# Optimization experiments

Hardware: AMD Instinct MI355X
Metric: run time of the kernel (lower is better)

## Reference

```python
import jax, jax.numpy as jnp
import numpy as np

HEADS = 6
K = 3       # kernel_size
PAD = 1     # padding (stride = 1, so AvgPool is identity and h=H, w=W)


def setup_inputs() -> dict:
    key = jax.random.key(0)
    ks = jax.random.split(key, 6)
    B, H, W, C = 8, 56, 56, 192
    k4h = (K ** 4) * HEADS  # 486
    s = 0.02
    return {
        "x":  jax.random.normal(ks[0], (B, H, W, C), jnp.float32),
        # weights stored as (in, out), i.e. transpose of torch nn.Linear.weight
        "Wv": jax.random.normal(ks[1], (C, C), jnp.float32) * s,
        "Wa": jax.random.normal(ks[2], (C, k4h), jnp.float32) * s,
        "ba": jnp.zeros((k4h,), jnp.float32),
        "Wp": jax.random.normal(ks[3], (C, C), jnp.float32) * s,
        "bp": jnp.zeros((C,), jnp.float32),
    }


def _outlook(x, Wv, Wa, ba, Wp, bp):
    B, H, W, C = x.shape
    hd = C // HEADS
    scale = hd ** (-0.5)
    k2 = K * K
    hw = H * W

    # v projection (no bias), to NCHW
    v = jnp.einsum("bhwc,cd->bdhw", x, Wv)                       # [B,C,H,W]

    # unfold: extract k x k local windows (same ordering as nn.Unfold: C, ki, kj)
    vp = jnp.pad(v, ((0, 0), (0, 0), (PAD, PAD), (PAD, PAD)))
    patches = jnp.stack(
        [vp[:, :, i:i + H, j:j + W] for i in range(K) for j in range(K)],
        axis=2,
    )                                                            # [B,C,k2,H,W]
    v = patches.reshape(B, HEADS, hd, k2, hw).transpose(0, 1, 4, 3, 2)  # [B,h,hw,k2,hd]

    # attention weights: dense predicted per location (pool is identity, stride=1)
    a = x.reshape(B, hw, C) @ Wa + ba                            # [B,hw,heads*k2*k2]
    a = a.reshape(B, hw, HEADS, k2, k2).transpose(0, 2, 1, 3, 4)  # [B,h,hw,k2,k2]
    a = jax.nn.softmax(a * scale, axis=-1)

    out = jnp.einsum("bnpkq,bnpqd->bnpkd", a, v)                 # [B,h,hw,k2,hd]

    # fold (col2im): scatter-add overlapping windows back, stride=1
    cols = out.transpose(0, 1, 4, 3, 2).reshape(B, C, K, K, H, W)
    acc = jnp.zeros((B, C, H + 2 * PAD, W + 2 * PAD), x.dtype)
    for i in range(K):
        for j in range(K):
            acc = acc.at[:, :, i:i + H, j:j + W].add(cols[:, :, i, j])
    y = acc[:, :, PAD:PAD + H, PAD:PAD + W].transpose(0, 2, 3, 1)  # [B,H,W,C]

    return y @ Wp + bp


def reference(x, Wv, Wa, ba, Wp, bp):
    return _outlook(x, Wv, Wa, ba, Wp, bp)
```

## Files before the change

### kernel.cpp

```cpp
#include <hip/hip_runtime.h>
#include <hip/hip_bf16.h>
#include <cstdint>

#define DI __device__ __forceinline__

typedef __attribute__((ext_vector_type(8))) short short8;
typedef __attribute__((ext_vector_type(4))) float f32x4;

DI float bflo(uint32_t u) { return __builtin_bit_cast(float, (uint32_t)(u << 16)); }
DI float bfhi(uint32_t u) { return __builtin_bit_cast(float, (uint32_t)(u & 0xffff0000u)); }
DI uint32_t cvtpk(float lo, float hi) {
    uint32_t r;
    asm("v_cvt_pk_bf16_f32 %0, %1, %2" : "=v"(r) : "v"(lo), "v"(hi));
    return r;
}
DI void gload16(const void* g, void* s) {
    __builtin_amdgcn_global_load_lds(
        (const __attribute__((address_space(1))) uint32_t*)g,
        (__attribute__((address_space(3))) uint32_t*)s, 16, 0, 0);
}
DI int xcd_swizzle(int orig, int nwg) {
    const int q = nwg >> 3, r = nwg & 7;
    const int x = orig & 7, i = orig >> 3;
    return (x < r ? x * (q + 1) : r * (q + 1) + (x - r) * q) + i;
}

constexpr int BATCH = 8, HH_IMG = 56, WW_IMG = 56, C = 192;
constexpr int HEADS = 6, HD = 32, NA = 486;
constexpr int NAP = 528;
constexpr int MROWS = BATCH * HH_IMG * WW_IMG;
constexpr int KK = 192;
constexpr int TILE_B  = 49152;
constexpr int PANEL_B = 49152;
constexpr int WTB_B   = 73728;

__global__ __launch_bounds__(256) void prep_all(const float* __restrict__ x,
                                                const float* __restrict__ Wv,
                                                const float* __restrict__ Wa,
                                                const float* __restrict__ Wp,
                                                const float* __restrict__ ba,
                                                uint8_t* __restrict__ xbf,
                                                uint8_t* __restrict__ WT,
                                                uint8_t* __restrict__ WTB,
                                                float* __restrict__ baP) {
    const int bid = blockIdx.x;
    if (bid < 2352) {
        const int g = bid * 256 + threadIdx.x;
        const int m = g / 24, cc = g % 24;
        const int ks = cc >> 2, lg = cc & 3;
        const float* src = x + (size_t)m * KK + cc * 8;
        const float4 v0 = *(const float4*)src;
        const float4 v1 = *(const float4*)(src + 4);
        uint4 o;
        o.x = cvtpk(v0.x, v0.y); o.y = cvtpk(v0.z, v0.w);
        o.z = cvtpk(v1.x, v1.y); o.w = cvtpk(v1.z, v1.w);
        const size_t off = (size_t)(m >> 7) * PANEL_B +
                           ((((m >> 4) & 7) * 6 + ks) * 64 + (lg << 4) + (m & 15)) * 16;
        *(uint4*)(xbf + off) = o;
        return;
    }
    const int tid = (bid - 2352) * 256 + threadIdx.x;
    if (tid < 18432) {
        const int s = tid % 24, rem = tid / 24;
        const int p = rem & 127, tile = rem >> 7;
        const int lc = (p >> 5) * 32 + 2 * (p & 15) + ((p >> 4) & 1);
        const int u  = tile * 128 + lc;
        const float* src = nullptr; int nc = 0, col = 0;
        if (u < 192) { src = Wv; nc = 192; col = u; }
        else if (u < 720) {
            const int up = u - 192;
            const int head = up / 88, r88 = up - head * 88;
            if (r88 < 81) { src = Wa; nc = NA; col = head * 81 + r88; }
        }
        const int k0 = s * 8;
        uint32_t d[4];
#pragma unroll
        for (int e = 0; e < 4; ++e) {
            const float f0 = src ? src[(size_t)(k0 + 2 * e) * nc + col]     : 0.f;
            const float f1 = src ? src[(size_t)(k0 + 2 * e + 1) * nc + col] : 0.f;
            d[e] = cvtpk(f0, f1);
        }
        const int sb = (s * 16) ^ ((p & 7) << 4);
        *(uint4*)(WT + (size_t)tile * TILE_B + p * 384 + sb) =
            make_uint4(d[0], d[1], d[2], d[3]);
    } else if (tid < 18432 + 4608) {
        const int g = tid - 18432;
        const int l = g & 63, gg = g >> 6;
        const int ks = gg % 6, nrIdx = gg / 6;
        const int pp = nrIdx >> 1, h = nrIdx & 1;
        const int col = pp * 32 + 2 * (l & 15) + h;
        const int k0  = ks * 32 + (l >> 4) * 8;
        uint32_t d[4];
#pragma unroll
        for (int e = 0; e < 4; ++e) {
            const float f0 = Wp[(size_t)(k0 + 2 * e) * 192 + col];
            const float f1 = Wp[(size_t)(k0 + 2 * e + 1) * 192 + col];
            d[e] = cvtpk(f0, f1);
        }
        *(uint4*)(WTB + (size_t)g * 16) = make_uint4(d[0], d[1], d[2], d[3]);
    } else if (tid < 18432 + 4608 + NAP) {
        const int pc = tid - 18432 - 4608;
        const int head = pc / 88, r88 = pc - head * 88;
        baP[pc] = (r88 < 81) ? ba[head * 81 + r88] : 0.f;
    }
}

__global__ __launch_bounds__(256, 2) void gemm_fr(
    const uint8_t* __restrict__ Afr,
    const uint8_t* __restrict__ WT,
    uint16_t* __restrict__ zOut, uint16_t* __restrict__ alogP,
    const float* __restrict__ baP) {
    __shared__ __align__(16) uint8_t sm[TILE_B];
    const int t    = threadIdx.x;
    const int wgid = xcd_swizzle(blockIdx.x, gridDim.x);
    const int mg   = wgid / 6, ti = wgid - mg * 6;
    const int m0   = mg * 128;
    const int l    = t & 63, wid = t >> 6;
    const int wr   = wid >> 1, wc = wid & 1;
    const int lr   = l & 15, lg = l >> 4;

    const uint8_t* wt = WT + (size_t)ti * TILE_B;
#pragma unroll
    for (int i = 0; i < 12; ++i) {
        const int off = wid * 12288 + i * 1024;
        gload16(wt + off + l * 16, sm + off);
    }

    const uint8_t* ap = Afr + (size_t)mg * PANEL_B;
    short8 aR[6][4];
#pragma unroll
    for (int ks = 0; ks < 6; ++ks)
#pragma unroll
        for (int mr = 0; mr < 4; ++mr) {
            const int r = wr * 4 + mr;
            aR[ks][mr] = *(const short8*)(ap + (size_t)(((r * 6 + ks) * 64) + l) * 16);
        }
    __syncthreads();

    f32x4 acc[4][4];
#pragma unroll
    for (int mr = 0; mr < 4; ++mr)
#pragma unroll
        for (int nr = 0; nr < 4; ++nr) acc[mr][nr] = f32x4{0.f, 0.f, 0.f, 0.f};
#pragma unroll
    for (int ks = 0; ks < 6; ++ks) {
        const int cb = ks * 64 + lg * 16;
        short8 b[4];
#pragma unroll
        for (int nr = 0; nr < 4; ++nr) {
            const int rn = wc * 64 + nr * 16 + lr;
            b[nr] = *(const short8*)(sm + rn * 384 + (cb ^ ((rn & 7) << 4)));
        }
#pragma unroll
        for (int mr = 0; mr < 4; ++mr)
#pragma unroll
            for (int nr = 0; nr < 4; ++nr)
                acc[mr][nr] = __builtin_amdgcn_mfma_f32_16x16x32_bf16(
                    aR[ks][mr], b[nr], acc[mr][nr], 0, 0, 0);
    }

    const int gcol0 = ti * 128 + wc * 64;
#pragma unroll
    for (int pr = 0; pr < 2; ++pr) {
        const int uc = gcol0 + pr * 32 + 2 * lr;
        if (uc < 192) {
#pragma unroll
            for (int mr = 0; mr < 4; ++mr) {
                const size_t rb = (size_t)(m0 + wr * 64 + mr * 16 + lg * 4);
#pragma unroll
                for (int j = 0; j < 4; ++j)
                    *(uint32_t*)(zOut + (rb + j) * 192 + uc) =
                        cvtpk(acc[mr][2 * pr][j], acc[mr][2 * pr + 1][j]);
            }
        } else {
            const int pc = uc - 192;
            if (pc < NAP) {
                const float be = baP[pc], bo = baP[pc + 1];
#pragma unroll
                for (int mr = 0; mr < 4; ++mr) {
                    const size_t rb = (size_t)(m0 + wr * 64 + mr * 16 + lg * 4);
#pragma unroll
                    for (int j = 0; j < 4; ++j)
                        *(uint32_t*)(alogP + (rb + j) * NAP + pc) =
                            cvtpk(acc[mr][2 * pr][j] + be, acc[mr][2 * pr + 1][j] + bo);
                }
            }
        }
    }
}

constexpr int TH = 4, TW = 8;
constexpr int HALO_W = TW + 4;
constexpr int HSTR = 80;
constexpr int PXSTR = HEADS * HSTR;
constexpr int VL_BYTES = 96 * PXSTR;

__global__ __launch_bounds__(192) void attn_fused(const uint16_t* __restrict__ z,
                                                  const uint16_t* __restrict__ alogP,
                                                  const uint8_t* __restrict__ WTB,
                                                  const float* __restrict__ bp,
                                                  float* __restrict__ out) {
    __shared__ __align__(16) uint8_t smem[VL_BYTES];
    const int b   = blockIdx.z;
    const int ty0 = blockIdx.y * TH, tx0 = blockIdx.x * TW;
    const int t   = threadIdx.x;

#pragma unroll
    for (int it = 0; it < 12; ++it) {
        const int f  = t + it * 192;
        const int px = f / 24, c8 = f % 24;
        const int hy = px / HALO_W, hx = px % HALO_W;
        const int y = ty0 + hy - 2, x = tx0 + hx - 2;
        uint4 val = make_uint4(0u, 0u, 0u, 0u);
        if ((unsigned)y < HH_IMG && (unsigned)x < WW_IMG)
            val = *(const uint4*)&z[(((size_t)b * HH_IMG + y) * WW_IMG + x) * C + c8 * 8];
        *(uint4*)(smem + px * PXSTR + (c8 >> 2) * HSTR + (c8 & 3) * 16) = val;
    }

    const int n   = t % HEADS, pxl = t / HEADS;
    const int py  = pxl >> 3, px_ = pxl & 7;
    const int Py  = ty0 + py, Px = tx0 + px_;
    const float scl2 = 0.17677669529663687f * 1.4426950408889634f;

    float cw[5][5] = {};
#pragma unroll
    for (int i = 0; i < 3; ++i)
#pragma unroll
        for (int j = 0; j < 3; ++j) {
            const int sy = Py - i + 1, sx = Px - j + 1;
            if ((unsigned)sy < HH_IMG && (unsigned)sx < WW_IMG) {
                const uint8_t* rp = (const uint8_t*)alogP +
                    (((size_t)b * HH_IMG + sy) * WW_IMG + sx) * (NAP * 2) + n * 176;
                const int win = i * 3 + j;
                const int off = win * 18, a0 = off & ~15, base = off - a0;
                const uint4 u0 = *(const uint4*)(rp + a0);
                const uint4 u1 = *(const uint4*)(rp + a0 + 16);
                const uint32_t dd[8] = {u0.x, u0.y, u0.z, u0.w, u1.x, u1.y, u1.z, u1.w};
                float w[9], s = 0.f;
#pragma unroll
                for (int q = 0; q < 9; ++q) {
                    const int bb = base + 2 * q;
                    const uint32_t dw = dd[bb >> 2];
                    const float f0 = (bb & 2) ? bfhi(dw) : bflo(dw);
                    w[q] = __builtin_amdgcn_exp2f(f0 * scl2);
                    s += w[q];
                }
                const float inv = __builtin_amdgcn_rcpf(s);
#pragma unroll
                for (int qi = 0; qi < 3; ++qi)
#pragma unroll
                    for (int qj = 0; qj < 3; ++qj)
                        cw[qi - i + 2][qj - j + 2] += w[qi * 3 + qj] * inv;
            }
        }
    __syncthreads();

    float acc[HD] = {};
#pragma unroll
    for (int dy = 0; dy < 5; ++dy)
#pragma unroll
        for (int dx = 0; dx < 5; ++dx) {
            const float wq = cw[dy][dx];
            const uint8_t* vp = smem + ((py + dy) * HALO_W + (px_ + dx)) * PXSTR + n * HSTR;
#pragma unroll
            for (int v8 = 0; v8 < 4; ++v8) {
                const uint4 raw = *(const uint4*)(vp + v8 * 16);
                const uint32_t r0 = raw.x, r1 = raw.y, r2 = raw.z, r3 = raw.w;
                acc[v8*8+0] = fmaf(wq, bflo(r0), acc[v8*8+0]);
                acc[v8*8+1] = fmaf(wq, bfhi(r0), acc[v8*8+1]);
                acc[v8*8+2] = fmaf(wq, bflo(r1), acc[v8*8+2]);
                acc[v8*8+3] = fmaf(wq, bfhi(r1), acc[v8*8+3]);
                acc[v8*8+4] = fmaf(wq, bflo(r2), acc[v8*8+4]);
                acc[v8*8+5] = fmaf(wq, bfhi(r2), acc[v8*8+5]);
                acc[v8*8+6] = fmaf(wq, bflo(r3), acc[v8*8+6]);
                acc[v8*8+7] = fmaf(wq, bfhi(r3), acc[v8*8+7]);
            }
        }
    __syncthreads();

    {
        uint8_t* pb = smem + pxl * 384;
        const int key = (pxl & 7) << 4;
#pragma unroll
        for (int g2 = 0; g2 < 4; ++g2) {
            uint4 o;
            o.x = cvtpk(acc[g2 * 8 + 0], acc[g2 * 8 + 1]);
            o.y = cvtpk(acc[g2 * 8 + 2], acc[g2 * 8 + 3]);
            o.z = cvtpk(acc[g2 * 8 + 4], acc[g2 * 8 + 5]);
            o.w = cvtpk(acc[g2 * 8 + 6], acc[g2 * 8 + 7]);
            *(uint4*)(pb + ((n * 64 + g2 * 16) ^ key)) = o;
        }
    }
    __syncthreads();

    const int l = t & 63, wid = t >> 6;
    const int lr = l & 15, lg = l >> 4;
    short8 aF[2][6];
#pragma unroll
    for (int r = 0; r < 2; ++r)
#pragma unroll
        for (int ks = 0; ks < 6; ++ks) {
            const int row = r * 16 + lr;
            aF[r][ks] = *(const short8*)(smem + row * 384 +
                          ((ks * 64 + lg * 16) ^ ((row & 7) << 4)));
        }
    f32x4 gacc[2][4];
#pragma unroll
    for (int r = 0; r < 2; ++r)
#pragma unroll
        for (int f = 0; f < 4; ++f) gacc[r][f] = f32x4{0.f, 0.f, 0.f, 0.f};
#pragma unroll
    for (int ks = 0; ks < 6; ++ks) {
        short8 bF[4];
#pragma unroll
        for (int f = 0; f < 4; ++f) {
            const int nrIdx = wid * 4 + f;
            bF[f] = *(const short8*)(WTB + (size_t)(((nrIdx * 6 + ks) * 64) + l) * 16);
        }
#pragma unroll
        for (int r = 0; r < 2; ++r)
#pragma unroll
            for (int f = 0; f < 4; ++f)
                gacc[r][f] = __builtin_amdgcn_mfma_f32_16x16x32_bf16(
                    aF[r][ks], bF[f], gacc[r][f], 0, 0, 0);
    }

#pragma unroll
    for (int pi = 0; pi < 2; ++pi) {
        const int col = wid * 64 + pi * 32 + 2 * lr;
        const float be = bp[col], bo = bp[col + 1];
#pragma unroll
        for (int r = 0; r < 2; ++r)
#pragma unroll
            for (int j = 0; j < 4; ++j) {
                const int prow = r * 16 + lg * 4 + j;
                const int gy = ty0 + (prow >> 3), gx = tx0 + (prow & 7);
                float* op = out + (((size_t)b * HH_IMG + gy) * WW_IMG + gx) * C + col;
                *(float2*)op = make_float2(gacc[r][2 * pi][j] + be,
                                           gacc[r][2 * pi + 1][j] + bo);
            }
    }
}

extern "C" void kernel_launch(void* const* d_in, const int* in_sizes, int n_in,
                              void* d_out, int out_size, void* d_ws, size_t ws_size,
                              hipStream_t stream) {
    const float* x  = (const float*)d_in[0];
    const float* Wv = (const float*)d_in[1];
    const float* Wa = (const float*)d_in[2];
    const float* ba = (const float*)d_in[3];
    const float* Wp = (const float*)d_in[4];
    const float* bp = (const float*)d_in[5];
    float* out = (float*)d_out;

    uint16_t* z     = (uint16_t*)d_ws;
    uint16_t* alogP = z + (size_t)MROWS * C;
    uint8_t*  xbf   = (uint8_t*)(alogP + (size_t)MROWS * NAP);
    uint8_t*  WT    = xbf + (size_t)(MROWS / 128) * PANEL_B;
    uint8_t*  WTB   = WT + 6 * (size_t)TILE_B;
    float*    baP   = (float*)(WTB + WTB_B);

    prep_all<<<2352 + 93, 256, 0, stream>>>(x, Wv, Wa, Wp, ba, xbf, WT, WTB, baP);
    gemm_fr<<<(MROWS / 128) * 6, 256, 0, stream>>>(xbf, WT, z, alogP, baP);
    attn_fused<<<dim3(WW_IMG / TW, HH_IMG / TH, BATCH), dim3(192), 0, stream>>>(
        z, alogP, WTB, bp, out);
}
```

Before: 60.74 us.

## Store attention logits as FP8 with per-head padding to 96 bytes

The attention-logit intermediate that gemm_fr writes and attn_fused reads is now stored as FP8 (e4m3) instead of bf16, with each head padded to 96 entries (576 per pixel). The goal is to roughly halve the global-memory traffic for this large intermediate, which is read nine times per pixel by neighbours. The padding also lets the GEMM's N dimension exactly fill its column tiles (768 = 6×128), which removes the bound check. The risk is reduced precision in the softmax logits, which could push results outside tolerance, and the byte-wide writes are narrower stores.

After: 56.84 us. 6.4% less time.

```diff
diff --git a/kernel.cpp b/kernel.cpp
--- a/kernel.cpp
+++ b/kernel.cpp
@@ -14,6 +14,31 @@
     asm("v_cvt_pk_bf16_f32 %0, %1, %2" : "=v"(r) : "v"(lo), "v"(hi));
     return r;
 }
+#if __has_builtin(__builtin_amdgcn_cvt_pk_fp8_f32)
+DI uint32_t fp8pk(float a, float b) {
+    return (uint32_t)__builtin_amdgcn_cvt_pk_fp8_f32(a, b, 0, false);
+}
+#else
+DI uint32_t fp8pk(float a, float b) {
+    uint32_t r;
+    asm("v_cvt_pk_fp8_f32 %0, %1, %2" : "=v"(r) : "v"(a), "v"(b));
+    return r;
+}
+#endif
+#if __has_builtin(__builtin_amdgcn_cvt_f32_fp8)
+#define FP8DEC(dw, sel) __builtin_amdgcn_cvt_f32_fp8((dw), (sel))
+#else
+DI float fp8dec_(uint32_t dw, int sel) {
+    const uint32_t u = (dw >> (8 * sel)) & 0xFFu;
+    const uint32_t s = (u & 0x80u) << 24;
+    const uint32_t em = u & 0x7Fu;
+    float mag;
+    if (em >= 8) mag = __builtin_bit_cast(float, (((em >> 3) + 120u) << 23) | ((em & 7u) << 20));
+    else         mag = (float)em * 0.001953125f;
+    return __builtin_bit_cast(float, s | __builtin_bit_cast(uint32_t, mag));
+}
+#define FP8DEC(dw, sel) fp8dec_((dw), (sel))
+#endif
 DI void gload16(const void* g, void* s) {
     __builtin_amdgcn_global_load_lds(
         (const __attribute__((address_space(1))) uint32_t*)g,
@@ -27,7 +52,8 @@
 
 constexpr int BATCH = 8, HH_IMG = 56, WW_IMG = 56, C = 192;
 constexpr int HEADS = 6, HD = 32, NA = 486;
-constexpr int NAP = 528;
+constexpr int NAPB = 576;
+constexpr int HSTA = 96;
 constexpr int MROWS = BATCH * HH_IMG * WW_IMG;
 constexpr int KK = 192;
 constexpr int TILE_B  = 49152;
@@ -67,10 +93,10 @@
         const int u  = tile * 128 + lc;
         const float* src = nullptr; int nc = 0, col = 0;
         if (u < 192) { src = Wv; nc = 192; col = u; }
-        else if (u < 720) {
+        else {
             const int up = u - 192;
-            const int head = up / 88, r88 = up - head * 88;
-            if (r88 < 81) { src = Wa; nc = NA; col = head * 81 + r88; }
+            const int head = up / HSTA, r96 = up - head * HSTA;
+            if (r96 < 81) { src = Wa; nc = NA; col = head * 81 + r96; }
         }
         const int k0 = s * 8;
         uint32_t d[4];
@@ -98,17 +124,17 @@
             d[e] = cvtpk(f0, f1);
         }
         *(uint4*)(WTB + (size_t)g * 16) = make_uint4(d[0], d[1], d[2], d[3]);
-    } else if (tid < 18432 + 4608 + NAP) {
+    } else if (tid < 18432 + 4608 + NAPB) {
         const int pc = tid - 18432 - 4608;
-        const int head = pc / 88, r88 = pc - head * 88;
-        baP[pc] = (r88 < 81) ? ba[head * 81 + r88] : 0.f;
+        const int head = pc / HSTA, r96 = pc - head * HSTA;
+        baP[pc] = (r96 < 81) ? ba[head * 81 + r96] : 0.f;
     }
 }
 
 __global__ __launch_bounds__(256, 2) void gemm_fr(
     const uint8_t* __restrict__ Afr,
     const uint8_t* __restrict__ WT,
-    uint16_t* __restrict__ zOut, uint16_t* __restrict__ alogP,
+    uint16_t* __restrict__ zOut, uint8_t* __restrict__ alogP,
     const float* __restrict__ baP) {
     __shared__ __align__(16) uint8_t sm[TILE_B];
     const int t    = threadIdx.x;
@@ -174,16 +200,15 @@
             }
         } else {
             const int pc = uc - 192;
-            if (pc < NAP) {
-                const float be = baP[pc], bo = baP[pc + 1];
-#pragma unroll
-                for (int mr = 0; mr < 4; ++mr) {
-                    const size_t rb = (size_t)(m0 + wr * 64 + mr * 16 + lg * 4);
-#pragma unroll
-                    for (int j = 0; j < 4; ++j)
-                        *(uint32_t*)(alogP + (rb + j) * NAP + pc) =
-                            cvtpk(acc[mr][2 * pr][j] + be, acc[mr][2 * pr + 1][j] + bo);
-                }
+            const float be = baP[pc], bo = baP[pc + 1];
+#pragma unroll
+            for (int mr = 0; mr < 4; ++mr) {
+                const size_t rb = (size_t)(m0 + wr * 64 + mr * 16 + lg * 4);
+#pragma unroll
+                for (int j = 0; j < 4; ++j)
+                    *(uint16_t*)(alogP + (rb + j) * NAPB + pc) =
+                        (uint16_t)fp8pk(acc[mr][2 * pr][j] + be,
+                                        acc[mr][2 * pr + 1][j] + bo);
             }
         }
     }
@@ -195,8 +220,28 @@
 constexpr int PXSTR = HEADS * HSTR;
 constexpr int VL_BYTES = 96 * PXSTR;
 
+template <int I, int J>
+DI void wincoef(const uint8_t* __restrict__ rp, float (&cw)[5][5]) {
+    constexpr int OFF = (I * 3 + J) * 9, A0 = OFF & ~15, BASE = OFF - A0;
+    const uint4 u0 = *(const uint4*)(rp + A0);
+    const uint4 u1 = *(const uint4*)(rp + A0 + 16);
+    const uint32_t dd[8] = {u0.x, u0.y, u0.z, u0.w, u1.x, u1.y, u1.z, u1.w};
+    constexpr float scl2 = 0.17677669529663687f * 1.4426950408889634f;
+    float w[9], s = 0.f;
+#define DECQ(Q) w[Q] = __builtin_amdgcn_exp2f(                                 \
+        FP8DEC(dd[(BASE + Q) >> 2], (BASE + Q) & 3) * scl2); s += w[Q];
+    DECQ(0) DECQ(1) DECQ(2) DECQ(3) DECQ(4) DECQ(5) DECQ(6) DECQ(7) DECQ(8)
+#undef DECQ
+    const float inv = __builtin_amdgcn_rcpf(s);
+#pragma unroll
+    for (int qi = 0; qi < 3; ++qi)
+#pragma unroll
+        for (int qj = 0; qj < 3; ++qj)
+            cw[qi - I + 2][qj - J + 2] += w[qi * 3 + qj] * inv;
+}
+
 __global__ __launch_bounds__(192) void attn_fused(const uint16_t* __restrict__ z,
-                                                  const uint16_t* __restrict__ alogP,
+                                                  const uint8_t* __restrict__ alogP,
                                                   const uint8_t* __restrict__ WTB,
                                                   const float* __restrict__ bp,
                                                   float* __restrict__ out) {
@@ -220,39 +265,20 @@
     const int n   = t % HEADS, pxl = t / HEADS;
     const int py  = pxl >> 3, px_ = pxl & 7;
     const int Py  = ty0 + py, Px = tx0 + px_;
-    const float scl2 = 0.17677669529663687f * 1.4426950408889634f;
 
     float cw[5][5] = {};
-#pragma unroll
-    for (int i = 0; i < 3; ++i)
-#pragma unroll
-        for (int j = 0; j < 3; ++j) {
-            const int sy = Py - i + 1, sx = Px - j + 1;
-            if ((unsigned)sy < HH_IMG && (unsigned)sx < WW_IMG) {
-                const uint8_t* rp = (const uint8_t*)alogP +
-                    (((size_t)b * HH_IMG + sy) * WW_IMG + sx) * (NAP * 2) + n * 176;
-                const int win = i * 3 + j;
-                const int off = win * 18, a0 = off & ~15, base = off - a0;
-                const uint4 u0 = *(const uint4*)(rp + a0);
-                const uint4 u1 = *(const uint4*)(rp + a0 + 16);
-                const uint32_t dd[8] = {u0.x, u0.y, u0.z, u0.w, u1.x, u1.y, u1.z, u1.w};
-                float w[9], s = 0.f;
-#pragma unroll
-                for (int q = 0; q < 9; ++q) {
-                    const int bb = base + 2 * q;
-                    const uint32_t dw = dd[bb >> 2];
-                    const float f0 = (bb & 2) ? bfhi(dw) : bflo(dw);
-                    w[q] = __builtin_amdgcn_exp2f(f0 * scl2);
-                    s += w[q];
-                }
-                const float inv = __builtin_amdgcn_rcpf(s);
-#pragma unroll
-                for (int qi = 0; qi < 3; ++qi)
-#pragma unroll
-                    for (int qj = 0; qj < 3; ++qj)
-                        cw[qi - i + 2][qj - j + 2] += w[qi * 3 + qj] * inv;
-            }
-        }
+#define WINCALL(I_, J_)                                                        \
+    {                                                                          \
+        const int sy = Py - I_ + 1, sx = Px - J_ + 1;                          \
+        if ((unsigned)sy < HH_IMG && (unsigned)sx < WW_IMG)                    \
+            wincoef<I_, J_>(alogP +                                            \
+                (((size_t)b * HH_IMG + sy) * WW_IMG + sx) * NAPB + n * HSTA,   \
+                cw);                                                           \
+    }
+    WINCALL(0, 0) WINCALL(0, 1) WINCALL(0, 2)
+    WINCALL(1, 0) WINCALL(1, 1) WINCALL(1, 2)
+    WINCALL(2, 0) WINCALL(2, 1) WINCALL(2, 2)
+#undef WINCALL
     __syncthreads();
 
     float acc[HD] = {};
@@ -354,8 +380,8 @@
     float* out = (float*)d_out;
 
     uint16_t* z     = (uint16_t*)d_ws;
-    uint16_t* alogP = z + (size_t)MROWS * C;
-    uint8_t*  xbf   = (uint8_t*)(alogP + (size_t)MROWS * NAP);
+    uint8_t*  alogP = (uint8_t*)(z + (size_t)MROWS * C);
+    uint8_t*  xbf   = alogP + (size_t)MROWS * NAPB;
     uint8_t*  WT    = xbf + (size_t)(MROWS / 128) * PANEL_B;
     uint8_t*  WTB   = WT + 6 * (size_t)TILE_B;
     float*    baP   = (float*)(WTB + WTB_B);
```
